# Optimization experiments

Measured on AMD Instinct MI355X. Metric: run time of the kernel, lower is better.

The kernel has to match this reference:

```python
import jax, jax.numpy as jnp
import numpy as np

NUM_EXPERTS = 16


def setup_inputs() -> dict:
    key = jax.random.key(0)
    g, s, d = 2, 4096, 1024
    input = jax.random.normal(key, (g, s, d), dtype=jnp.float32)
    return {"input": input}


def reference(input):
    g, s, _ = input.shape
    E = NUM_EXPERTS
    assert s % E == 0
    capacity = 2 * s // E
    i = jnp.arange(s)
    expert = i % E          # round-robin expert assignment
    c = i // E              # capacity slot within expert
    # one-hot dispatch tensor [g, s, E, capacity], identical for every group
    output = jnp.zeros((g, s, E, capacity), dtype=input.dtype)
    output = output.at[:, i, expert, c].set(1.0)
    return (0.0, output, output.astype(jnp.bool_))
```

## Files before the change

### kernel.cpp

```cpp
#include <hip/hip_runtime.h>


#define N1   67108864u
#define NTOT 134217729u

__global__ void __launch_bounds__(256) rr_gate_ones(float* __restrict__ out) {
    const unsigned tid = blockIdx.x * blockDim.x + threadIdx.x;
    const unsigned i   = tid & 4095u;
    const unsigned g   = (tid >> 12) & 1u;
    const unsigned t   = tid >> 13;
    const unsigned hot = ((i & 15u) << 9) | (i >> 4);
    const unsigned p   = 1u + t * N1 + g * 33554432u + i * 8192u + hot;
    out[p] = 1.0f;
}

extern "C" void kernel_launch(void* const* d_in, const int* in_sizes, int n_in,
                              void* d_out, int out_size, void* d_ws, size_t ws_size,
                              hipStream_t stream) {
    (void)d_in; (void)in_sizes; (void)n_in; (void)d_ws; (void)ws_size; (void)out_size;
    float* out = (float*)d_out;
    hipMemsetAsync(d_out, 0, (size_t)NTOT * sizeof(float), stream);
    hipLaunchKernelGGL(rr_gate_ones, dim3(64), dim3(256), 0, stream, out);
}
```

Baseline: 93.42 us.

## Fuse zero-fill and one-hot scatter into a single vectorized write kernel

Drops the separate hipMemsetAsync plus scatter kernel. One kernel now writes every output row in full with float4 stores, putting the single 1.0 in place as it goes. The one-element offset of the leading scalar is handled by shifting the hot index, so rows stay 16-byte aligned. The aim is to write the large buffer once in a single pass and skip a second launch. The risk is that each thread's 8 consecutive float4 stores give a lane-strided pattern that may coalesce worse than memset.

```diff
diff --git a/kernel.cpp b/kernel.cpp
--- a/kernel.cpp
+++ b/kernel.cpp
@@ -1,24 +1,48 @@
 #include <hip/hip_runtime.h>
 
 
-#define N1   67108864u
-#define NTOT 134217729u
+#define NROWS 16384u
+#define ROWS_PER_BLOCK 8u
+#define NBLOCKS 2048u
 
-__global__ void __launch_bounds__(256) rr_gate_ones(float* __restrict__ out) {
-    const unsigned tid = blockIdx.x * blockDim.x + threadIdx.x;
-    const unsigned i   = tid & 4095u;
-    const unsigned g   = (tid >> 12) & 1u;
-    const unsigned t   = tid >> 13;
-    const unsigned hot = ((i & 15u) << 9) | (i >> 4);
-    const unsigned p   = 1u + t * N1 + g * 33554432u + i * 8192u + hot;
-    out[p] = 1.0f;
+__global__ void __launch_bounds__(256) rr_gate_fused(float4* __restrict__ out4,
+                                                     float* __restrict__ out) {
+    const unsigned tid = threadIdx.x;
+    const unsigned r0  = blockIdx.x * ROWS_PER_BLOCK;
+    const float4 zero = make_float4(0.0f, 0.0f, 0.0f, 0.0f);
+
+    for (unsigned rr = 0; rr < ROWS_PER_BLOCK; ++rr) {
+        const unsigned r = r0 + rr;
+        const unsigned i   = r & 4095u;
+        const unsigned hot = ((i & 15u) << 9) | (i >> 4);
+        const unsigned hl  = hot + 1u;
+        const unsigned qh  = hl >> 2;
+        const unsigned ht  = qh >> 3;
+        const unsigned sl  = qh & 7u;
+        const unsigned comp = hl & 3u;
+        float4 hv;
+        hv.x = (comp == 0u) ? 1.0f : 0.0f;
+        hv.y = (comp == 1u) ? 1.0f : 0.0f;
+        hv.z = (comp == 2u) ? 1.0f : 0.0f;
+        hv.w = (comp == 3u) ? 1.0f : 0.0f;
+
+        float4* base = out4 + ((size_t)r << 11) + (size_t)tid * 8u;
+        const bool own = (tid == ht);
+#pragma unroll
+        for (unsigned k = 0; k < 8u; ++k) {
+            float4 v = (own && k == sl) ? hv : zero;
+            base[k] = v;
+        }
+    }
+    if (blockIdx.x == 0 && tid == 0) {
+        out[134217728u] = 0.0f;
+    }
 }
 
 extern "C" void kernel_launch(void* const* d_in, const int* in_sizes, int n_in,
                               void* d_out, int out_size, void* d_ws, size_t ws_size,
                               hipStream_t stream) {
     (void)d_in; (void)in_sizes; (void)n_in; (void)d_ws; (void)ws_size; (void)out_size;
-    float* out = (float*)d_out;
-    hipMemsetAsync(d_out, 0, (size_t)NTOT * sizeof(float), stream);
-    hipLaunchKernelGGL(rr_gate_ones, dim3(64), dim3(256), 0, stream, out);
+    hipLaunchKernelGGL(rr_gate_fused, dim3(NBLOCKS), dim3(256), 0, stream,
+                       (float4*)d_out, (float*)d_out);
 }
```

New measurement: 157.7 us. +68.8%, slower.

## Fuse zero-fill and one-hot scatter into a single vectorized nontemporal fill kernel

Applied to the files above, without the earlier changes.

Replaces the hipMemsetAsync plus scattered one-hot store kernel with one kernel. It writes every output float4 exactly once, putting 1.0 in the right lane when the row's hot index falls in that quad, and uses nontemporal stores. This removes the second launch and the re-touch of cache lines after the memset. It relies on hand-derived index math for the leading scalar offset, and the trailing element gets its own store.

```diff
diff --git a/kernel.cpp b/kernel.cpp
--- a/kernel.cpp
+++ b/kernel.cpp
@@ -1,24 +1,43 @@
 #include <hip/hip_runtime.h>
 
 
-#define N1   67108864u
-#define NTOT 134217729u
+typedef float floatx4 __attribute__((ext_vector_type(4)));
 
-__global__ void __launch_bounds__(256) rr_gate_ones(float* __restrict__ out) {
-    const unsigned tid = blockIdx.x * blockDim.x + threadIdx.x;
-    const unsigned i   = tid & 4095u;
-    const unsigned g   = (tid >> 12) & 1u;
-    const unsigned t   = tid >> 13;
-    const unsigned hot = ((i & 15u) << 9) | (i >> 4);
-    const unsigned p   = 1u + t * N1 + g * 33554432u + i * 8192u + hot;
-    out[p] = 1.0f;
+#define NQ     33554432u
+#define NTHR   (2048u * 256u)
+
+__global__ void __launch_bounds__(256) rr_gate_fill(floatx4* __restrict__ out4,
+                                                    float* __restrict__ out) {
+    const unsigned t  = blockIdx.x * 256u + threadIdx.x;
+    const unsigned ql = t & 2047u;
+    unsigned r        = t >> 11;
+    floatx4* p        = out4 + t;
+
+#pragma unroll 8
+    for (unsigned it = 0; it < 64u; ++it) {
+        const unsigned i  = r & 4095u;
+        const unsigned hl = (((i & 15u) << 9) | (i >> 4)) + 1u;
+        floatx4 v = (floatx4)(0.0f);
+        if (ql == (hl >> 2)) {
+            const unsigned comp = hl & 3u;
+            v.x = (comp == 0u) ? 1.0f : 0.0f;
+            v.y = (comp == 1u) ? 1.0f : 0.0f;
+            v.z = (comp == 2u) ? 1.0f : 0.0f;
+            v.w = (comp == 3u) ? 1.0f : 0.0f;
+        }
+        __builtin_nontemporal_store(v, p);
+        p += NTHR;
+        r += 256u;
+    }
+    if (t == 0) {
+        out[134217728u] = 0.0f;
+    }
 }
 
 extern "C" void kernel_launch(void* const* d_in, const int* in_sizes, int n_in,
                               void* d_out, int out_size, void* d_ws, size_t ws_size,
                               hipStream_t stream) {
     (void)d_in; (void)in_sizes; (void)n_in; (void)d_ws; (void)ws_size; (void)out_size;
-    float* out = (float*)d_out;
-    hipMemsetAsync(d_out, 0, (size_t)NTOT * sizeof(float), stream);
-    hipLaunchKernelGGL(rr_gate_ones, dim3(64), dim3(256), 0, stream, out);
+    hipLaunchKernelGGL(rr_gate_fill, dim3(2048), dim3(256), 0, stream,
+                       (floatx4*)d_out, (float*)d_out);
 }
```

Result: slower. 118.6 us (+26.9%).
